# Kernel optimization log

Hardware: AMD Instinct MI355X
Metric: run time of the kernel (lower is better)

Reference implementation:

```python
import jax, jax.numpy as jnp
import numpy as np
import math

B, S, E, H, DK = 2, 2048, 1024, 16, 64  # batch, seq, embed, heads, d_k (= n_wires)

def setup_inputs() -> dict:
    key = jax.random.key(0)
    k1, k2, k3, k4, k5 = jax.random.split(key, 5)
    scale = 0.02
    return {
        "x": jax.random.normal(k1, (B, S, E), dtype=jnp.float32),
        "Wk": jax.random.normal(k2, (E, E), dtype=jnp.float32) * scale,
        "Wv": jax.random.normal(k3, (E, E), dtype=jnp.float32) * scale,
        "Wq": jax.random.normal(k4, (H, DK, E), dtype=jnp.float32) * scale,
        "theta": jax.random.normal(k5, (DK,), dtype=jnp.float32) * scale,
    }

def reference(x, Wk, Wv, Wq, theta):
    batch, seq, embed = x.shape
    n_heads, d_k = Wq.shape[0], Wq.shape[1]
    # K, V projections (nn.Linear, no bias): x @ W.T
    k = (x @ Wk.T).reshape(batch, seq, n_heads, d_k).transpose(0, 2, 1, 3)  # [B,H,S,dk]
    v = (x @ Wv.T).reshape(batch, seq, n_heads, d_k).transpose(0, 2, 1, 3)  # [B,H,S,dk]
    # Quantum query path: per-head linear proj -> RX(proj_i) then RX(theta_i) on wire i from |0>,
    # MeasureAll(PauliZ) on independent wires gives <Z_i> = cos(proj_i + theta_i) exactly.
    proj = jnp.einsum('bse,hde->bhsd', x, Wq)          # [B,H,S,dk]
    q = jnp.cos(proj + theta)                           # [B,H,S,dk]
    scores = jnp.einsum('bhsd,bhtd->bhst', q, k) / math.sqrt(d_k)  # [B,H,S,S]
    attn = jax.nn.softmax(scores, axis=-1)
    out = jnp.einsum('bhst,bhtd->bhsd', attn, v)        # [B,H,S,dk]
    return out.transpose(0, 2, 1, 3).reshape(batch, seq, embed)
```

## Files before the change

kernel.cpp:

```cpp
#include <hip/hip_runtime.h>
#include <hip/hip_bf16.h>

constexpr int B  = 2;
constexpr int S  = 2048;
constexpr int E  = 1024;
constexpr int H  = 16;
constexpr int DK = 64;
constexpr int M  = B * S;
constexpr int N3 = 3 * E;
constexpr long RSZ = (long)B * H * S * DK;

#define QSCALE 0.18033688011112042f

using bf16x8 = __attribute__((ext_vector_type(8))) __bf16;
using bf16x4 = __attribute__((ext_vector_type(4))) __bf16;
using f32x4  = __attribute__((ext_vector_type(4))) float;

__device__ __forceinline__ void async16(__bf16* lds, const __bf16* g) {
    __builtin_amdgcn_global_load_lds(
        (const __attribute__((address_space(1))) void*)g,
        (__attribute__((address_space(3))) void*)lds, 16, 0, 0);
}

__global__ __launch_bounds__(256)
void cvt_kernel(const float* __restrict__ x, const float* __restrict__ Wk,
                const float* __restrict__ Wv, const float* __restrict__ Wq,
                __bf16* __restrict__ xb, __bf16* __restrict__ wall) {
    const long e = ((long)blockIdx.x * 256 + threadIdx.x) * 4;
    const float* src;
    __bf16* dst;
    if (e < (long)M * E) { src = x + e; dst = xb + e; }
    else {
        const long e2 = e - (long)M * E;
        const int which = (int)(e2 >> 20);
        const long off  = e2 & ((1L << 20) - 1);
        src = (which == 0 ? Wk : which == 1 ? Wv : Wq) + off;
        dst = wall + e2;
    }
    float4 f = *reinterpret_cast<const float4*>(src);
    bf16x4 o;
    o[0] = (__bf16)f.x; o[1] = (__bf16)f.y; o[2] = (__bf16)f.z; o[3] = (__bf16)f.w;
    *reinterpret_cast<bf16x4*>(dst) = o;
}

__global__ __launch_bounds__(256, 3)
void qkv_gemm(const __bf16* __restrict__ xb, const __bf16* __restrict__ wall,
              const float* __restrict__ theta, __bf16* __restrict__ kvq) {
    __shared__ __align__(1024) __bf16 smem[6 * 128 * 32];
    __bf16* tile = smem;

    const int t    = threadIdx.x;
    const int lane = t & 63;
    const int w    = t >> 6;
    const int quad = lane >> 4;
    const int l16  = lane & 15;
    const int wm   = w >> 1, wn = w & 1;
    const int mbase = blockIdx.y * 128;
    const int nbase = blockIdx.x * 128;

    f32x4 acc[4][4];
    #pragma unroll
    for (int i = 0; i < 4; i++)
        #pragma unroll
        for (int j = 0; j < 4; j++)
            acc[i][j] = f32x4{0.f, 0.f, 0.f, 0.f};

    const int srow = lane >> 2;
    const int srcc = (lane & 3) ^ ((lane >> 3) & 3);
    const __bf16* ga = xb   + (long)(mbase + srow) * E + srcc * 8;
    const __bf16* gb = wall + (long)(nbase + srow) * E + srcc * 8;

    const int csw = (l16 >> 1) & 3;

    #pragma unroll
    for (int pt = 0; pt < 2; pt++) {
        #pragma unroll
        for (int c = 0; c < 2; c++) {
            async16(smem + pt * 4096 +         (c * 64 + w * 16) * 32,
                    ga + (long)(c * 64 + w * 16) * E + pt * 32);
            async16(smem + pt * 4096 + 12288 + (c * 64 + w * 16) * 32,
                    gb + (long)(c * 64 + w * 16) * E + pt * 32);
        }
    }

    int cur = 0;
    constexpr int ITERS = E / 32;
    for (int it = 0; it < ITERS; it++) {
        if (it < ITERS - 1) asm volatile("s_waitcnt vmcnt(4)" ::: "memory");
        else                asm volatile("s_waitcnt vmcnt(0)" ::: "memory");
        asm volatile("s_barrier" ::: "memory");

        if (it + 2 < ITERS) {
            const int pb  = (cur == 0) ? 2 : cur - 1;
            const int kk2 = (it + 2) * 32;
            #pragma unroll
            for (int c = 0; c < 2; c++) {
                async16(smem + pb * 4096 +         (c * 64 + w * 16) * 32,
                        ga + (long)(c * 64 + w * 16) * E + kk2);
                async16(smem + pb * 4096 + 12288 + (c * 64 + w * 16) * 32,
                        gb + (long)(c * 64 + w * 16) * E + kk2);
            }
        }

        const __bf16* Asb = smem + cur * 4096;
        const __bf16* Bsb = smem + cur * 4096 + 12288;
        bf16x8 a[4], b[4];
        #pragma unroll
        for (int i = 0; i < 4; i++)
            a[i] = *reinterpret_cast<const bf16x8*>(
                &Asb[(wm * 64 + i * 16 + l16) * 32 + (quad ^ csw) * 8]);
        #pragma unroll
        for (int j = 0; j < 4; j++)
            b[j] = *reinterpret_cast<const bf16x8*>(
                &Bsb[(wn * 64 + j * 16 + l16) * 32 + (quad ^ csw) * 8]);
        #pragma unroll
        for (int i = 0; i < 4; i++)
            #pragma unroll
            for (int j = 0; j < 4; j++)
                acc[i][j] = __builtin_amdgcn_mfma_f32_16x16x32_bf16(a[i], b[j], acc[i][j], 0, 0, 0);

        cur = (cur == 2) ? 0 : cur + 1;
    }

    const int region = nbase >> 10;
    const int bb = mbase >> 11;
    if (region == 1) {
        __syncthreads();
        #pragma unroll
        for (int i = 0; i < 4; i++) {
            const int cchunk = wm * 8 + i * 2 + (quad >> 1);
            #pragma unroll
            for (int j = 0; j < 4; j++) {
                const int cirb = wn * 64 + j * 16 + l16;
                const int cs = cchunk ^ l16;
                bf16x4 pk;
                #pragma unroll
                for (int r = 0; r < 4; r++) pk[r] = (__bf16)acc[i][j][r];
                *reinterpret_cast<bf16x4*>(&tile[cirb * 128 + cs * 8 + (quad & 1) * 4]) = pk;
            }
        }
        __syncthreads();
        const int h0 = (nbase & 1023) >> 6;
        __bf16* vt = kvq + RSZ;
        #pragma unroll
        for (int p = 0; p < 8; p++) {
            const int dcol = p * 16 + (t >> 4);
            const int lc = t & 15;
            const int cs2 = lc ^ (dcol & 15);
            bf16x8 vv = *reinterpret_cast<const bf16x8*>(&tile[dcol * 128 + cs2 * 8]);
            const int hh = h0 + (dcol >> 6), d = dcol & 63;
            *reinterpret_cast<bf16x8*>(
                &vt[((long)(bb * H + hh) * DK + d) * S + (mbase & 2047) + lc * 8]) = vv;
        }
    } else {
        __bf16* dst = kvq + (region == 2 ? 2 * RSZ : 0);
        float th[4];
        if (region == 2) {
            #pragma unroll
            for (int j = 0; j < 4; j++) th[j] = theta[j * 16 + l16];
        }
        #pragma unroll
        for (int i = 0; i < 4; i++) {
            const int row0 = mbase + wm * 64 + i * 16 + quad * 4;
            #pragma unroll
            for (int j = 0; j < 4; j++) {
                const int cir = (nbase & 1023) + wn * 64 + j * 16 + l16;
                const int h = cir >> 6, d = cir & 63;
                #pragma unroll
                for (int r = 0; r < 4; r++) {
                    const int s = (row0 + r) & 2047;
                    float v = acc[i][j][r];
                    if (region == 2) v = cosf(v + th[j]) * QSCALE;
                    dst[((long)(bb * H + h) * S + s) * DK + d] = (__bf16)v;
                }
            }
        }
    }
}

__global__ __launch_bounds__(256, 2)
void attn_kernel(const __bf16* __restrict__ q_ws, const __bf16* __restrict__ k_ws,
                 const __bf16* __restrict__ v_ws, float* __restrict__ out) {
    __shared__ __align__(1024) __bf16 Ks[3][64 * 64];
    __shared__ __align__(1024) __bf16 Vs[3][64 * 64];
    __shared__ __align__(16)   __bf16 Pl[4][32 * 72];
    __shared__ __align__(16)   float  ls_lds[4][32];

    const int lane = threadIdx.x & 63;
    const int w    = threadIdx.x >> 6;
    const int quad = lane >> 4;
    const int l16  = lane & 15;

    const int id    = blockIdx.x;
    const int bh    = (id & 7) + 8 * ((id >> 3) & 3);
    const int qbase = (id >> 5) * 128 + w * 32;

    const __bf16* qp = q_ws + (long)bh * S * DK;
    const __bf16* kp = k_ws + (long)bh * S * DK;
    const __bf16* vp = v_ws + (long)bh * DK * S;

    const int sr  = lane >> 3;
    const int scs = (lane & 7) ^ sr;

    bf16x8 bq[2][2];
    #pragma unroll
    for (int nt = 0; nt < 2; nt++)
        #pragma unroll
        for (int ks = 0; ks < 2; ks++)
            bq[nt][ks] = *reinterpret_cast<const bf16x8*>(
                qp + (long)(qbase + nt * 16 + l16) * DK + ks * 32 + quad * 8);

    f32x4 o[2][4];
    #pragma unroll
    for (int i = 0; i < 2; i++)
        #pragma unroll
        for (int j = 0; j < 4; j++) o[i][j] = f32x4{0.f, 0.f, 0.f, 0.f};
    float lsum[2] = {0.f, 0.f};

    #pragma unroll
    for (int pt = 0; pt < 2; pt++) {
        #pragma unroll
        for (int i = 0; i < 2; i++) {
            const int row = w * 16 + i * 8;
            async16(&Ks[pt][row * 64], kp + (long)(pt * 64 + row + sr) * DK + scs * 8);
            async16(&Vs[pt][row * 64], vp + (long)(row + sr) * S + pt * 64 + scs * 8);
        }
    }

    int cur = 0;
    constexpr int ITERS = S / 64;
    for (int it = 0; it < ITERS; it++) {
        if (it < ITERS - 1) asm volatile("s_waitcnt vmcnt(4)" ::: "memory");
        else                asm volatile("s_waitcnt vmcnt(0)" ::: "memory");
        asm volatile("s_barrier" ::: "memory");

        if (it + 2 < ITERS) {
            const int kt2 = (it + 2) * 64;
            const int pb  = (cur == 0) ? 2 : cur - 1;
            #pragma unroll
            for (int i = 0; i < 2; i++) {
                const int row = w * 16 + i * 8;
                async16(&Ks[pb][row * 64], kp + (long)(kt2 + row + sr) * DK + scs * 8);
                async16(&Vs[pb][row * 64], vp + (long)(row + sr) * S + kt2 + scs * 8);
            }
        }

        f32x4 sacc[4][2];
        #pragma unroll
        for (int i = 0; i < 4; i++)
            #pragma unroll
            for (int j = 0; j < 2; j++) sacc[i][j] = f32x4{0.f, 0.f, 0.f, 0.f};
        #pragma unroll
        for (int ks = 0; ks < 2; ks++) {
            bf16x8 ak[4];
            #pragma unroll
            for (int mt = 0; mt < 4; mt++)
                ak[mt] = *reinterpret_cast<const bf16x8*>(
                    &Ks[cur][(mt * 16 + l16) * 64 + ((ks * 4 + quad) ^ (l16 & 7)) * 8]);
            #pragma unroll
            for (int mt = 0; mt < 4; mt++)
                #pragma unroll
                for (int nt = 0; nt < 2; nt++)
                    sacc[mt][nt] = __builtin_amdgcn_mfma_f32_16x16x32_bf16(
                        ak[mt], bq[nt][ks], sacc[mt][nt], 0, 0, 0);
        }

        #pragma unroll
        for (int mt = 0; mt < 4; mt++)
            #pragma unroll
            for (int nt = 0; nt < 2; nt++) {
                float p0 = __builtin_amdgcn_exp2f(sacc[mt][nt][0]);
                float p1 = __builtin_amdgcn_exp2f(sacc[mt][nt][1]);
                float p2 = __builtin_amdgcn_exp2f(sacc[mt][nt][2]);
                float p3 = __builtin_amdgcn_exp2f(sacc[mt][nt][3]);
                lsum[nt] += (p0 + p1) + (p2 + p3);
                bf16x4 pk;
                pk[0] = (__bf16)p0; pk[1] = (__bf16)p1;
                pk[2] = (__bf16)p2; pk[3] = (__bf16)p3;
                *reinterpret_cast<bf16x4*>(
                    &Pl[w][(nt * 16 + l16) * 72 + mt * 16 + quad * 4]) = pk;
            }

        #pragma unroll
        for (int kh = 0; kh < 2; kh++) {
            bf16x8 bv[4];
            #pragma unroll
            for (int nt = 0; nt < 4; nt++)
                bv[nt] = *reinterpret_cast<const bf16x8*>(
                    &Vs[cur][(nt * 16 + l16) * 64 + ((kh * 4 + quad) ^ (l16 & 7)) * 8]);
            #pragma unroll
            for (int mt = 0; mt < 2; mt++) {
                bf16x8 ap = *reinterpret_cast<const bf16x8*>(
                    &Pl[w][(mt * 16 + l16) * 72 + kh * 32 + quad * 8]);
                #pragma unroll
                for (int nt = 0; nt < 4; nt++)
                    o[mt][nt] = __builtin_amdgcn_mfma_f32_16x16x32_bf16(
                        ap, bv[nt], o[mt][nt], 0, 0, 0);
            }
        }

        cur = (cur == 2) ? 0 : cur + 1;
    }

    #pragma unroll
    for (int nt = 0; nt < 2; nt++) {
        float v = lsum[nt];
        v += __shfl_xor(v, 16);
        v += __shfl_xor(v, 32);
        ls_lds[w][nt * 16 + l16] = v;
    }

    const int b = bh >> 4, h = bh & 15;
    #pragma unroll
    for (int mt = 0; mt < 2; mt++) {
        f32x4 lv = *reinterpret_cast<const f32x4*>(&ls_lds[w][mt * 16 + quad * 4]);
        #pragma unroll
        for (int r = 0; r < 4; r++) {
            const float inv = 1.0f / lv[r];
            const int srow = qbase + mt * 16 + quad * 4 + r;
            #pragma unroll
            for (int nt = 0; nt < 4; nt++)
                out[(long)(b * S + srow) * E + h * DK + nt * 16 + l16] = o[mt][nt][r] * inv;
        }
    }
}

__device__ inline bf16x8 cvt_frag(const float* __restrict__ p) {
    float4 f0 = *reinterpret_cast<const float4*>(p);
    float4 f1 = *reinterpret_cast<const float4*>(p + 4);
    bf16x8 r;
    r[0] = (__bf16)f0.x; r[1] = (__bf16)f0.y; r[2] = (__bf16)f0.z; r[3] = (__bf16)f0.w;
    r[4] = (__bf16)f1.x; r[5] = (__bf16)f1.y; r[6] = (__bf16)f1.z; r[7] = (__bf16)f1.w;
    return r;
}
template <int MODE>
__global__ __launch_bounds__(256, 2)
void proj_kernel(const float* __restrict__ x, const float* __restrict__ W,
                 const float* __restrict__ theta, __bf16* __restrict__ out) {
    const int lane = threadIdx.x & 63;
    const int w    = threadIdx.x >> 6;
    const int quad = lane >> 4;
    const int l16  = lane & 15;
    const int mbase = blockIdx.y * 128 + w * 32;
    const int nbase = blockIdx.x * 128;
    f32x4 acc[2][8];
    #pragma unroll
    for (int i = 0; i < 2; i++)
        #pragma unroll
        for (int j = 0; j < 8; j++) acc[i][j] = f32x4{0.f, 0.f, 0.f, 0.f};
    float th[4];
    if (MODE == 2) {
        #pragma unroll
        for (int j = 0; j < 4; j++) th[j] = theta[j * 16 + l16];
    }
    for (int kk = 0; kk < E; kk += 32) {
        bf16x8 a[2], b[8];
        #pragma unroll
        for (int mt = 0; mt < 2; mt++)
            a[mt] = cvt_frag(x + (long)(mbase + mt * 16 + l16) * E + kk + quad * 8);
        #pragma unroll
        for (int nt = 0; nt < 8; nt++)
            b[nt] = cvt_frag(W + (long)(nbase + nt * 16 + l16) * E + kk + quad * 8);
        #pragma unroll
        for (int mt = 0; mt < 2; mt++)
            #pragma unroll
            for (int nt = 0; nt < 8; nt++)
                acc[mt][nt] = __builtin_amdgcn_mfma_f32_16x16x32_bf16(a[mt], b[nt], acc[mt][nt], 0, 0, 0);
    }
    #pragma unroll
    for (int mt = 0; mt < 2; mt++) {
        const int row0 = mbase + mt * 16 + quad * 4;
        #pragma unroll
        for (int nt = 0; nt < 8; nt++) {
            const int col = nbase + nt * 16 + l16;
            const int h = col >> 6, d = col & 63;
            #pragma unroll
            for (int r = 0; r < 4; r++) {
                const int row = row0 + r;
                const int bb = row >> 11, s = row & 2047;
                float v = acc[mt][nt][r];
                if (MODE == 2) v = cosf(v + th[nt & 3]) * QSCALE;
                long idx;
                if (MODE == 1) idx = ((long)(bb * H + h) * DK + d) * S + s;
                else           idx = ((long)(bb * H + h) * S + s) * DK + d;
                out[idx] = (__bf16)v;
            }
        }
    }
}

extern "C" void kernel_launch(void* const* d_in, const int* in_sizes, int n_in,
                              void* d_out, int out_size, void* d_ws, size_t ws_size,
                              hipStream_t stream) {
    const float* x     = (const float*)d_in[0];
    const float* Wk    = (const float*)d_in[1];
    const float* Wv    = (const float*)d_in[2];
    const float* Wq    = (const float*)d_in[3];
    const float* theta = (const float*)d_in[4];
    float* out = (float*)d_out;

    __bf16* kvq  = (__bf16*)d_ws;
    __bf16* xb   = kvq + 3 * RSZ;
    __bf16* wall = xb + (long)M * E;
    __bf16* k_ws = kvq;
    __bf16* v_t  = kvq + RSZ;
    __bf16* q_ws = kvq + 2 * RSZ;

    const size_t need = (3 * RSZ + (long)M * E + (long)N3 * E) * 2;
    dim3 blk(256);
    if (ws_size >= need) {
        cvt_kernel<<<dim3(7168), blk, 0, stream>>>(x, Wk, Wv, Wq, xb, wall);
        qkv_gemm<<<dim3(N3 / 128, M / 128), blk, 0, stream>>>(xb, wall, theta, kvq);
    } else {
        dim3 gp(E / 128, M / 128);
        proj_kernel<0><<<gp, blk, 0, stream>>>(x, Wk, nullptr, k_ws);
        proj_kernel<1><<<gp, blk, 0, stream>>>(x, Wv, nullptr, v_t);
        proj_kernel<2><<<gp, blk, 0, stream>>>(x, Wq, theta, q_ws);
    }

    attn_kernel<<<dim3(512), blk, 0, stream>>>(q_ws, k_ws, v_t, out);
}
```

Before: 173.1 us.

## Software-pipeline PV matmul one tile behind QK in attention loop

Restructures the attention main loop so the P·V MFMAs for the previous key tile run after the current tile's QK^T MFMAs and before its exp, with P double-buffered per wave and V triple-buffered. K moves to a double buffer, and prefetch distance drops from two tiles ahead to one, with a full vmcnt(0) wait each iteration. The aim is to give the scheduler independent MFMA work to overlap with the exp/convert and LDS store latency. In exchange, latency hiding for global loads is shorter and LDS usage grows from the extra P buffer.

```diff
diff --git a/kernel.cpp b/kernel.cpp
--- a/kernel.cpp
+++ b/kernel.cpp
@@ -181,9 +181,9 @@
 __global__ __launch_bounds__(256, 2)
 void attn_kernel(const __bf16* __restrict__ q_ws, const __bf16* __restrict__ k_ws,
                  const __bf16* __restrict__ v_ws, float* __restrict__ out) {
-    __shared__ __align__(1024) __bf16 Ks[3][64 * 64];
+    __shared__ __align__(1024) __bf16 Ks[2][64 * 64];
     __shared__ __align__(1024) __bf16 Vs[3][64 * 64];
-    __shared__ __align__(16)   __bf16 Pl[4][32 * 72];
+    __shared__ __align__(16)   __bf16 Pl[4][2][32 * 72];
     __shared__ __align__(16)   float  ls_lds[4][32];
 
     const int lane = threadIdx.x & 63;
@@ -217,31 +217,49 @@
         for (int j = 0; j < 4; j++) o[i][j] = f32x4{0.f, 0.f, 0.f, 0.f};
     float lsum[2] = {0.f, 0.f};
 
-    #pragma unroll
-    for (int pt = 0; pt < 2; pt++) {
-        #pragma unroll
-        for (int i = 0; i < 2; i++) {
-            const int row = w * 16 + i * 8;
-            async16(&Ks[pt][row * 64], kp + (long)(pt * 64 + row + sr) * DK + scs * 8);
-            async16(&Vs[pt][row * 64], vp + (long)(row + sr) * S + pt * 64 + scs * 8);
-        }
-    }
-
-    int cur = 0;
+    auto pv_step = [&](const __bf16* Vsrc, const __bf16* Psrc) {
+        #pragma unroll
+        for (int kh = 0; kh < 2; kh++) {
+            bf16x8 bv[4];
+            #pragma unroll
+            for (int nt = 0; nt < 4; nt++)
+                bv[nt] = *reinterpret_cast<const bf16x8*>(
+                    &Vsrc[(nt * 16 + l16) * 64 + ((kh * 4 + quad) ^ (l16 & 7)) * 8]);
+            #pragma unroll
+            for (int mt = 0; mt < 2; mt++) {
+                bf16x8 ap = *reinterpret_cast<const bf16x8*>(
+                    &Psrc[(mt * 16 + l16) * 72 + kh * 32 + quad * 8]);
+                #pragma unroll
+                for (int nt = 0; nt < 4; nt++)
+                    o[mt][nt] = __builtin_amdgcn_mfma_f32_16x16x32_bf16(
+                        ap, bv[nt], o[mt][nt], 0, 0, 0);
+            }
+        }
+    };
+
+    #pragma unroll
+    for (int i = 0; i < 2; i++) {
+        const int row = w * 16 + i * 8;
+        async16(&Ks[0][row * 64], kp + (long)(row + sr) * DK + scs * 8);
+        async16(&Vs[0][row * 64], vp + (long)(row + sr) * S + scs * 8);
+    }
+
+    int kcur = 0, vcur = 0, pcur = 0;
     constexpr int ITERS = S / 64;
     for (int it = 0; it < ITERS; it++) {
-        if (it < ITERS - 1) asm volatile("s_waitcnt vmcnt(4)" ::: "memory");
-        else                asm volatile("s_waitcnt vmcnt(0)" ::: "memory");
+        asm volatile("s_waitcnt vmcnt(0)" ::: "memory");
         asm volatile("s_barrier" ::: "memory");
 
-        if (it + 2 < ITERS) {
-            const int kt2 = (it + 2) * 64;
-            const int pb  = (cur == 0) ? 2 : cur - 1;
+        const int vprv = (vcur == 0) ? 2 : vcur - 1;
+
+        if (it + 1 < ITERS) {
+            const int kt1  = (it + 1) * 64;
+            const int vnxt = (vcur == 2) ? 0 : vcur + 1;
             #pragma unroll
             for (int i = 0; i < 2; i++) {
                 const int row = w * 16 + i * 8;
-                async16(&Ks[pb][row * 64], kp + (long)(kt2 + row + sr) * DK + scs * 8);
-                async16(&Vs[pb][row * 64], vp + (long)(row + sr) * S + kt2 + scs * 8);
+                async16(&Ks[kcur ^ 1][row * 64], kp + (long)(kt1 + row + sr) * DK + scs * 8);
+                async16(&Vs[vnxt][row * 64], vp + (long)(row + sr) * S + kt1 + scs * 8);
             }
         }
 
@@ -256,7 +274,7 @@
             #pragma unroll
             for (int mt = 0; mt < 4; mt++)
                 ak[mt] = *reinterpret_cast<const bf16x8*>(
-                    &Ks[cur][(mt * 16 + l16) * 64 + ((ks * 4 + quad) ^ (l16 & 7)) * 8]);
+                    &Ks[kcur][(mt * 16 + l16) * 64 + ((ks * 4 + quad) ^ (l16 & 7)) * 8]);
             #pragma unroll
             for (int mt = 0; mt < 4; mt++)
                 #pragma unroll
@@ -264,6 +282,8 @@
                     sacc[mt][nt] = __builtin_amdgcn_mfma_f32_16x16x32_bf16(
                         ak[mt], bq[nt][ks], sacc[mt][nt], 0, 0, 0);
         }
+
+        if (it) pv_step(&Vs[vprv][0], &Pl[w][pcur ^ 1][0]);
 
         #pragma unroll
         for (int mt = 0; mt < 4; mt++)
@@ -278,28 +298,17 @@
                 pk[0] = (__bf16)p0; pk[1] = (__bf16)p1;
                 pk[2] = (__bf16)p2; pk[3] = (__bf16)p3;
                 *reinterpret_cast<bf16x4*>(
-                    &Pl[w][(nt * 16 + l16) * 72 + mt * 16 + quad * 4]) = pk;
-            }
-
-        #pragma unroll
-        for (int kh = 0; kh < 2; kh++) {
-            bf16x8 bv[4];
-            #pragma unroll
-            for (int nt = 0; nt < 4; nt++)
-                bv[nt] = *reinterpret_cast<const bf16x8*>(
-                    &Vs[cur][(nt * 16 + l16) * 64 + ((kh * 4 + quad) ^ (l16 & 7)) * 8]);
-            #pragma unroll
-            for (int mt = 0; mt < 2; mt++) {
-                bf16x8 ap = *reinterpret_cast<const bf16x8*>(
-                    &Pl[w][(mt * 16 + l16) * 72 + kh * 32 + quad * 8]);
-                #pragma unroll
-                for (int nt = 0; nt < 4; nt++)
-                    o[mt][nt] = __builtin_amdgcn_mfma_f32_16x16x32_bf16(
-                        ap, bv[nt], o[mt][nt], 0, 0, 0);
-            }
-        }
-
-        cur = (cur == 2) ? 0 : cur + 1;
+                    &Pl[w][pcur][(nt * 16 + l16) * 72 + mt * 16 + quad * 4]) = pk;
+            }
+
+        kcur ^= 1;
+        pcur ^= 1;
+        vcur = (vcur == 2) ? 0 : vcur + 1;
+    }
+
+    {
+        const int vprv = (vcur == 0) ? 2 : vcur - 1;
+        pv_step(&Vs[vprv][0], &Pl[w][pcur ^ 1][0]);
     }
 
     #pragma unroll
```

After: 170.8 us. Within noise of the previous version (-1.4%).

## Load K/V tiles directly from global into registers, dropping LDS staging

Applied to the files above, without the earlier changes.

The attention kernel stops staging K and V tiles through shared memory with async global-to-LDS copies, triple buffering and barriers. Each wave now reads its K and V fragments straight from global memory into registers, double-buffering K one tile ahead. This removes the LDS traffic and the per-iteration block barrier. In exchange, the four waves of a block each fetch the same K/V tiles from global memory, relying on cache for reuse, register pressure rises, and V latency is only partly hidden.

```diff
diff --git a/kernel.cpp b/kernel.cpp
--- a/kernel.cpp
+++ b/kernel.cpp
@@ -181,10 +181,8 @@
 __global__ __launch_bounds__(256, 2)
 void attn_kernel(const __bf16* __restrict__ q_ws, const __bf16* __restrict__ k_ws,
                  const __bf16* __restrict__ v_ws, float* __restrict__ out) {
-    __shared__ __align__(1024) __bf16 Ks[3][64 * 64];
-    __shared__ __align__(1024) __bf16 Vs[3][64 * 64];
-    __shared__ __align__(16)   __bf16 Pl[4][32 * 72];
-    __shared__ __align__(16)   float  ls_lds[4][32];
+    __shared__ __align__(16) __bf16 Pl[4][32 * 72];
+    __shared__ __align__(16) float  ls_lds[4][32];
 
     const int lane = threadIdx.x & 63;
     const int w    = threadIdx.x >> 6;
@@ -199,8 +197,8 @@
     const __bf16* kp = k_ws + (long)bh * S * DK;
     const __bf16* vp = v_ws + (long)bh * DK * S;
 
-    const int sr  = lane >> 3;
-    const int scs = (lane & 7) ^ sr;
+    const __bf16* kbase = kp + (long)l16 * DK + quad * 8;
+    const __bf16* vbase = vp + (long)l16 * S  + quad * 8;
 
     bf16x8 bq[2][2];
     #pragma unroll
@@ -217,33 +215,29 @@
         for (int j = 0; j < 4; j++) o[i][j] = f32x4{0.f, 0.f, 0.f, 0.f};
     float lsum[2] = {0.f, 0.f};
 
-    #pragma unroll
-    for (int pt = 0; pt < 2; pt++) {
-        #pragma unroll
-        for (int i = 0; i < 2; i++) {
-            const int row = w * 16 + i * 8;
-            async16(&Ks[pt][row * 64], kp + (long)(pt * 64 + row + sr) * DK + scs * 8);
-            async16(&Vs[pt][row * 64], vp + (long)(row + sr) * S + pt * 64 + scs * 8);
-        }
-    }
-
-    int cur = 0;
     constexpr int ITERS = S / 64;
-    for (int it = 0; it < ITERS; it++) {
-        if (it < ITERS - 1) asm volatile("s_waitcnt vmcnt(4)" ::: "memory");
-        else                asm volatile("s_waitcnt vmcnt(0)" ::: "memory");
-        asm volatile("s_barrier" ::: "memory");
-
-        if (it + 2 < ITERS) {
-            const int kt2 = (it + 2) * 64;
-            const int pb  = (cur == 0) ? 2 : cur - 1;
-            #pragma unroll
-            for (int i = 0; i < 2; i++) {
-                const int row = w * 16 + i * 8;
-                async16(&Ks[pb][row * 64], kp + (long)(kt2 + row + sr) * DK + scs * 8);
-                async16(&Vs[pb][row * 64], vp + (long)(row + sr) * S + kt2 + scs * 8);
-            }
-        }
+
+    auto load_k = [&](bf16x8 (&kf)[8], int kt) {
+        #pragma unroll
+        for (int mt = 0; mt < 4; mt++)
+            #pragma unroll
+            for (int ks = 0; ks < 2; ks++)
+                kf[mt * 2 + ks] = *reinterpret_cast<const bf16x8*>(
+                    kbase + (long)(kt + mt * 16) * DK + ks * 32);
+    };
+
+    auto body = [&](bf16x8 (&kc)[8], bf16x8 (&kn)[8], int it) {
+        const int kt = it * 64;
+
+        bf16x8 vf[8];
+        #pragma unroll
+        for (int nt = 0; nt < 4; nt++)
+            #pragma unroll
+            for (int kh = 0; kh < 2; kh++)
+                vf[nt * 2 + kh] = *reinterpret_cast<const bf16x8*>(
+                    vbase + (long)(nt * 16) * S + kt + kh * 32);
+
+        if (it + 1 < ITERS) load_k(kn, kt + 64);
 
         f32x4 sacc[4][2];
         #pragma unroll
@@ -251,19 +245,13 @@
             #pragma unroll
             for (int j = 0; j < 2; j++) sacc[i][j] = f32x4{0.f, 0.f, 0.f, 0.f};
         #pragma unroll
-        for (int ks = 0; ks < 2; ks++) {
-            bf16x8 ak[4];
-            #pragma unroll
-            for (int mt = 0; mt < 4; mt++)
-                ak[mt] = *reinterpret_cast<const bf16x8*>(
-                    &Ks[cur][(mt * 16 + l16) * 64 + ((ks * 4 + quad) ^ (l16 & 7)) * 8]);
+        for (int ks = 0; ks < 2; ks++)
             #pragma unroll
             for (int mt = 0; mt < 4; mt++)
                 #pragma unroll
                 for (int nt = 0; nt < 2; nt++)
                     sacc[mt][nt] = __builtin_amdgcn_mfma_f32_16x16x32_bf16(
-                        ak[mt], bq[nt][ks], sacc[mt][nt], 0, 0, 0);
-        }
+                        kc[mt * 2 + ks], bq[nt][ks], sacc[mt][nt], 0, 0, 0);
 
         #pragma unroll
         for (int mt = 0; mt < 4; mt++)
@@ -282,12 +270,7 @@
             }
 
         #pragma unroll
-        for (int kh = 0; kh < 2; kh++) {
-            bf16x8 bv[4];
-            #pragma unroll
-            for (int nt = 0; nt < 4; nt++)
-                bv[nt] = *reinterpret_cast<const bf16x8*>(
-                    &Vs[cur][(nt * 16 + l16) * 64 + ((kh * 4 + quad) ^ (l16 & 7)) * 8]);
+        for (int kh = 0; kh < 2; kh++)
             #pragma unroll
             for (int mt = 0; mt < 2; mt++) {
                 bf16x8 ap = *reinterpret_cast<const bf16x8*>(
@@ -295,11 +278,15 @@
                 #pragma unroll
                 for (int nt = 0; nt < 4; nt++)
                     o[mt][nt] = __builtin_amdgcn_mfma_f32_16x16x32_bf16(
-                        ap, bv[nt], o[mt][nt], 0, 0, 0);
-            }
-        }
-
-        cur = (cur == 2) ? 0 : cur + 1;
+                        ap, vf[nt * 2 + kh], o[mt][nt], 0, 0, 0);
+            }
+    };
+
+    bf16x8 kf0[8], kf1[8];
+    load_k(kf0, 0);
+    for (int it = 0; it < ITERS; it += 2) {
+        body(kf0, kf1, it);
+        body(kf1, kf0, it + 1);
     }
 
     #pragma unroll
```

Result: slower. 240.4 us (+38.9%).

## Fuse fp32-to-bf16 conversion into QKV GEMM with register-staged double buffering

Applied to the files above, without the earlier changes.

The separate conversion kernel that wrote bf16 copies of x and the weights is removed. The QKV GEMM now loads fp32 directly into registers, converts to bf16, and writes a swizzled LDS tile, using a two-buffer register-prefetch pipeline in place of the three-stage async global-to-LDS pipeline. This drops one kernel launch and the round trip through the bf16 workspace. In exchange, the GEMM reads twice as many bytes per tile, performs the conversion inside its main loop, and x is converted again by every column block.

```diff
diff --git a/kernel.cpp b/kernel.cpp
--- a/kernel.cpp
+++ b/kernel.cpp
@@ -22,31 +22,11 @@
         (__attribute__((address_space(3))) void*)lds, 16, 0, 0);
 }
 
-__global__ __launch_bounds__(256)
-void cvt_kernel(const float* __restrict__ x, const float* __restrict__ Wk,
-                const float* __restrict__ Wv, const float* __restrict__ Wq,
-                __bf16* __restrict__ xb, __bf16* __restrict__ wall) {
-    const long e = ((long)blockIdx.x * 256 + threadIdx.x) * 4;
-    const float* src;
-    __bf16* dst;
-    if (e < (long)M * E) { src = x + e; dst = xb + e; }
-    else {
-        const long e2 = e - (long)M * E;
-        const int which = (int)(e2 >> 20);
-        const long off  = e2 & ((1L << 20) - 1);
-        src = (which == 0 ? Wk : which == 1 ? Wv : Wq) + off;
-        dst = wall + e2;
-    }
-    float4 f = *reinterpret_cast<const float4*>(src);
-    bf16x4 o;
-    o[0] = (__bf16)f.x; o[1] = (__bf16)f.y; o[2] = (__bf16)f.z; o[3] = (__bf16)f.w;
-    *reinterpret_cast<bf16x4*>(dst) = o;
-}
-
 __global__ __launch_bounds__(256, 3)
-void qkv_gemm(const __bf16* __restrict__ xb, const __bf16* __restrict__ wall,
-              const float* __restrict__ theta, __bf16* __restrict__ kvq) {
-    __shared__ __align__(1024) __bf16 smem[6 * 128 * 32];
+void qkv_fused(const float* __restrict__ x, const float* __restrict__ Wk,
+               const float* __restrict__ Wv, const float* __restrict__ Wq,
+               const float* __restrict__ theta, __bf16* __restrict__ kvq) {
+    __shared__ __align__(1024) __bf16 smem[4 * 4096];
     __bf16* tile = smem;
 
     const int t    = threadIdx.x;
@@ -65,45 +45,54 @@
         for (int j = 0; j < 4; j++)
             acc[i][j] = f32x4{0.f, 0.f, 0.f, 0.f};
 
-    const int srow = lane >> 2;
-    const int srcc = (lane & 3) ^ ((lane >> 3) & 3);
-    const __bf16* ga = xb   + (long)(mbase + srow) * E + srcc * 8;
-    const __bf16* gb = wall + (long)(nbase + srow) * E + srcc * 8;
-
-    const int csw = (l16 >> 1) & 3;
-
-    #pragma unroll
-    for (int pt = 0; pt < 2; pt++) {
+    const int sr  = t >> 1;
+    const int cg  = (t & 1) * 2;
+    const int key = (sr >> 1) & 3;
+    const float* asrc = x + (long)(mbase + sr) * E;
+    const int brow = nbase + sr;
+    const float* wsel = (brow >> 10) == 0 ? Wk : (brow >> 10) == 1 ? Wv : Wq;
+    const float* bsrc = wsel + (long)(brow & 1023) * E;
+
+    float4 ra[2][2], rb[2][2];
+    auto load_step = [&](int kk) {
         #pragma unroll
         for (int c = 0; c < 2; c++) {
-            async16(smem + pt * 4096 +         (c * 64 + w * 16) * 32,
-                    ga + (long)(c * 64 + w * 16) * E + pt * 32);
-            async16(smem + pt * 4096 + 12288 + (c * 64 + w * 16) * 32,
-                    gb + (long)(c * 64 + w * 16) * E + pt * 32);
-        }
-    }
-
-    int cur = 0;
+            const int lc = (cg + c) ^ key;
+            ra[c][0] = *reinterpret_cast<const float4*>(asrc + kk + lc * 8);
+            ra[c][1] = *reinterpret_cast<const float4*>(asrc + kk + lc * 8 + 4);
+            rb[c][0] = *reinterpret_cast<const float4*>(bsrc + kk + lc * 8);
+            rb[c][1] = *reinterpret_cast<const float4*>(bsrc + kk + lc * 8 + 4);
+        }
+    };
+    auto write_buf = [&](int buf) {
+        #pragma unroll
+        for (int c = 0; c < 2; c++) {
+            bf16x8 va, vb;
+            va[0] = (__bf16)ra[c][0].x; va[1] = (__bf16)ra[c][0].y;
+            va[2] = (__bf16)ra[c][0].z; va[3] = (__bf16)ra[c][0].w;
+            va[4] = (__bf16)ra[c][1].x; va[5] = (__bf16)ra[c][1].y;
+            va[6] = (__bf16)ra[c][1].z; va[7] = (__bf16)ra[c][1].w;
+            vb[0] = (__bf16)rb[c][0].x; vb[1] = (__bf16)rb[c][0].y;
+            vb[2] = (__bf16)rb[c][0].z; vb[3] = (__bf16)rb[c][0].w;
+            vb[4] = (__bf16)rb[c][1].x; vb[5] = (__bf16)rb[c][1].y;
+            vb[6] = (__bf16)rb[c][1].z; vb[7] = (__bf16)rb[c][1].w;
+            *reinterpret_cast<bf16x8*>(&smem[buf * 4096 + sr * 32 + (cg + c) * 8]) = va;
+            *reinterpret_cast<bf16x8*>(&smem[8192 + buf * 4096 + sr * 32 + (cg + c) * 8]) = vb;
+        }
+    };
+
+    load_step(0);
+    write_buf(0);
+    load_step(32);
+    asm volatile("s_waitcnt lgkmcnt(0)" ::: "memory");
+    asm volatile("s_barrier" ::: "memory");
+
     constexpr int ITERS = E / 32;
     for (int it = 0; it < ITERS; it++) {
-        if (it < ITERS - 1) asm volatile("s_waitcnt vmcnt(4)" ::: "memory");
-        else                asm volatile("s_waitcnt vmcnt(0)" ::: "memory");
-        asm volatile("s_barrier" ::: "memory");
-
-        if (it + 2 < ITERS) {
-            const int pb  = (cur == 0) ? 2 : cur - 1;
-            const int kk2 = (it + 2) * 32;
-            #pragma unroll
-            for (int c = 0; c < 2; c++) {
-                async16(smem + pb * 4096 +         (c * 64 + w * 16) * 32,
-                        ga + (long)(c * 64 + w * 16) * E + kk2);
-                async16(smem + pb * 4096 + 12288 + (c * 64 + w * 16) * 32,
-                        gb + (long)(c * 64 + w * 16) * E + kk2);
-            }
-        }
-
+        const int cur = it & 1;
         const __bf16* Asb = smem + cur * 4096;
-        const __bf16* Bsb = smem + cur * 4096 + 12288;
+        const __bf16* Bsb = smem + 8192 + cur * 4096;
+        const int csw = (l16 >> 1) & 3;
         bf16x8 a[4], b[4];
         #pragma unroll
         for (int i = 0; i < 4; i++)
@@ -119,7 +108,12 @@
             for (int j = 0; j < 4; j++)
                 acc[i][j] = __builtin_amdgcn_mfma_f32_16x16x32_bf16(a[i], b[j], acc[i][j], 0, 0, 0);
 
-        cur = (cur == 2) ? 0 : cur + 1;
+        if (it + 1 < ITERS) write_buf(cur ^ 1);
+        if (it + 2 < ITERS) load_step((it + 2) * 32);
+        if (it + 1 < ITERS) {
+            asm volatile("s_waitcnt lgkmcnt(0)" ::: "memory");
+            asm volatile("s_barrier" ::: "memory");
+        }
     }
 
     const int region = nbase >> 10;
@@ -325,70 +319,6 @@
     }
 }
 
-__device__ inline bf16x8 cvt_frag(const float* __restrict__ p) {
-    float4 f0 = *reinterpret_cast<const float4*>(p);
-    float4 f1 = *reinterpret_cast<const float4*>(p + 4);
-    bf16x8 r;
-    r[0] = (__bf16)f0.x; r[1] = (__bf16)f0.y; r[2] = (__bf16)f0.z; r[3] = (__bf16)f0.w;
-    r[4] = (__bf16)f1.x; r[5] = (__bf16)f1.y; r[6] = (__bf16)f1.z; r[7] = (__bf16)f1.w;
-    return r;
-}
-template <int MODE>
-__global__ __launch_bounds__(256, 2)
-void proj_kernel(const float* __restrict__ x, const float* __restrict__ W,
-                 const float* __restrict__ theta, __bf16* __restrict__ out) {
-    const int lane = threadIdx.x & 63;
-    const int w    = threadIdx.x >> 6;
-    const int quad = lane >> 4;
-    const int l16  = lane & 15;
-    const int mbase = blockIdx.y * 128 + w * 32;
-    const int nbase = blockIdx.x * 128;
-    f32x4 acc[2][8];
-    #pragma unroll
-    for (int i = 0; i < 2; i++)
-        #pragma unroll
-        for (int j = 0; j < 8; j++) acc[i][j] = f32x4{0.f, 0.f, 0.f, 0.f};
-    float th[4];
-    if (MODE == 2) {
-        #pragma unroll
-        for (int j = 0; j < 4; j++) th[j] = theta[j * 16 + l16];
-    }
-    for (int kk = 0; kk < E; kk += 32) {
-        bf16x8 a[2], b[8];
-        #pragma unroll
-        for (int mt = 0; mt < 2; mt++)
-            a[mt] = cvt_frag(x + (long)(mbase + mt * 16 + l16) * E + kk + quad * 8);
-        #pragma unroll
-        for (int nt = 0; nt < 8; nt++)
-            b[nt] = cvt_frag(W + (long)(nbase + nt * 16 + l16) * E + kk + quad * 8);
-        #pragma unroll
-        for (int mt = 0; mt < 2; mt++)
-            #pragma unroll
-            for (int nt = 0; nt < 8; nt++)
-                acc[mt][nt] = __builtin_amdgcn_mfma_f32_16x16x32_bf16(a[mt], b[nt], acc[mt][nt], 0, 0, 0);
-    }
-    #pragma unroll
-    for (int mt = 0; mt < 2; mt++) {
-        const int row0 = mbase + mt * 16 + quad * 4;
-        #pragma unroll
-        for (int nt = 0; nt < 8; nt++) {
-            const int col = nbase + nt * 16 + l16;
-            const int h = col >> 6, d = col & 63;
-            #pragma unroll
-            for (int r = 0; r < 4; r++) {
-                const int row = row0 + r;
-                const int bb = row >> 11, s = row & 2047;
-                float v = acc[mt][nt][r];
-                if (MODE == 2) v = cosf(v + th[nt & 3]) * QSCALE;
-                long idx;
-                if (MODE == 1) idx = ((long)(bb * H + h) * DK + d) * S + s;
-                else           idx = ((long)(bb * H + h) * S + s) * DK + d;
-                out[idx] = (__bf16)v;
-            }
-        }
-    }
-}
-
 extern "C" void kernel_launch(void* const* d_in, const int* in_sizes, int n_in,
                               void* d_out, int out_size, void* d_ws, size_t ws_size,
                               hipStream_t stream) {
@@ -400,23 +330,11 @@
     float* out = (float*)d_out;
 
     __bf16* kvq  = (__bf16*)d_ws;
-    __bf16* xb   = kvq + 3 * RSZ;
-    __bf16* wall = xb + (long)M * E;
     __bf16* k_ws = kvq;
     __bf16* v_t  = kvq + RSZ;
     __bf16* q_ws = kvq + 2 * RSZ;
 
-    const size_t need = (3 * RSZ + (long)M * E + (long)N3 * E) * 2;
     dim3 blk(256);
-    if (ws_size >= need) {
-        cvt_kernel<<<dim3(7168), blk, 0, stream>>>(x, Wk, Wv, Wq, xb, wall);
-        qkv_gemm<<<dim3(N3 / 128, M / 128), blk, 0, stream>>>(xb, wall, theta, kvq);
-    } else {
-        dim3 gp(E / 128, M / 128);
-        proj_kernel<0><<<gp, blk, 0, stream>>>(x, Wk, nullptr, k_ws);
-        proj_kernel<1><<<gp, blk, 0, stream>>>(x, Wv, nullptr, v_t);
-        proj_kernel<2><<<gp, blk, 0, stream>>>(x, Wq, theta, q_ws);
-    }
-
+    qkv_fused<<<dim3(N3 / 128, M / 128), blk, 0, stream>>>(x, Wk, Wv, Wq, theta, kvq);
     attn_kernel<<<dim3(512), blk, 0, stream>>>(q_ws, k_ws, v_t, out);
 }
```

Result: slower. 184.0 us (+6.3%).
